# Kernel optimization log

Measured on AMD Instinct MI355X. Metric: run time of the kernel, lower is better.

## Reference

```python
import jax, jax.numpy as jnp
import numpy as np

EMBED_DIM = 384
ROUTER_HIDDEN = 64
NUM_EXPERTS = 4
TOP_K = 1
TEMPERATURE = 2.0  # buffer value, clamp(min=0.1) is a no-op here
LN_EPS = 1e-5


def setup_inputs() -> dict:
    key = jax.random.key(0)
    kx, k1, k2 = jax.random.split(key, 3)
    x = jax.random.normal(kx, (16, 8192, EMBED_DIM), dtype=jnp.float32)
    ln_w = jnp.ones((EMBED_DIM,), dtype=jnp.float32)
    ln_b = jnp.zeros((EMBED_DIM,), dtype=jnp.float32)
    # kaiming-uniform-ish init, scale irrelevant for correctness testing
    w1 = jax.random.normal(k1, (EMBED_DIM, ROUTER_HIDDEN), dtype=jnp.float32) / np.sqrt(EMBED_DIM)
    w2 = jax.random.normal(k2, (ROUTER_HIDDEN, NUM_EXPERTS), dtype=jnp.float32) / np.sqrt(ROUTER_HIDDEN)
    return {"x": x, "ln_w": ln_w, "ln_b": ln_b, "w1": w1, "w2": w2}


def reference(x, ln_w, ln_b, w1, w2):
    T = jnp.maximum(jnp.float32(TEMPERATURE), 0.1)
    # LayerNorm over last dim
    mu = jnp.mean(x, axis=-1, keepdims=True)
    var = jnp.mean(jnp.square(x - mu), axis=-1, keepdims=True)
    h = (x - mu) * jax.lax.rsqrt(var + LN_EPS) * ln_w + ln_b
    # MLP gate: Linear(384->64, no bias) -> GELU(exact) -> Linear(64->4, no bias)
    h = jax.nn.gelu(jnp.einsum("bld,dh->blh", h, w1), approximate=False)
    logits = jnp.einsum("blh,he->ble", h, w2) / T
    probs = jax.nn.softmax(logits, axis=-1)  # (B, L, E)
    _, indices = jax.lax.top_k(probs, TOP_K)  # (B, L, top_k)
    B, L = indices.shape[0], indices.shape[1]
    # load-balance aux loss (f is non-differentiable, as under torch.no_grad)
    one_hot = jax.nn.one_hot(indices, NUM_EXPERTS, dtype=jnp.float32)  # (B, L, K, E)
    f = jnp.sum(one_hot, axis=(0, 1, 2)) / (B * L * TOP_K)  # (E,)
    P = jnp.mean(probs, axis=(0, 1))  # (E,)
    aux_loss = NUM_EXPERTS * jnp.sum(f * P)
    return probs, indices, aux_loss, probs
```

## Files before the change

### kernel.cpp

```cpp
#include <hip/hip_runtime.h>
#include <math.h>

#define EMBED 384
#define HID 64
#define NE 4
#define TPB 512
#define MT 8
#define JS 8
#define JPT 8
#define TOKB 512

#define WLN_F   (EMBED * HID)
#define W2_OFF  (WLN_F)
#define C1_OFF  (W2_OFF + HID * NE)
#define C2_OFF  (C1_OFF + HID)
#define PART_OFF (C2_OFF + HID)
#define RED_OFF (PART_OFF + 2 * TPB)
#define SMEM_FLOATS (RED_OFF + 2 * NE)

__global__ void
__attribute__((amdgpu_flat_work_group_size(TPB, TPB), amdgpu_waves_per_eu(2, 2)))
router_main(
    const float* __restrict__ x, const float* __restrict__ lnw,
    const float* __restrict__ lnb, const float* __restrict__ w1,
    const float* __restrict__ w2, float* __restrict__ out,
    float* __restrict__ ws, int ntok)
{
  extern __shared__ float smem[];
  float* wln = smem;
  float* w2s = smem + W2_OFF;
  float* c1s = smem + C1_OFF;
  float* c2s = smem + C2_OFF;
  float* part = smem + PART_OFF;
  float* red = smem + RED_OFF;

  const int tid = (int)threadIdx.x;

  {
    const float4* src = reinterpret_cast<const float4*>(w1);
    float4* dst = reinterpret_cast<float4*>(wln);
    #pragma unroll
    for (int k = 0; k < (WLN_F / 4) / TPB; ++k) {
      const int f4 = tid + k * TPB;
      const float sc = lnw[f4 >> 4];
      float4 v = src[f4];
      v.x *= sc; v.y *= sc; v.z *= sc; v.w *= sc;
      dst[f4] = v;
    }
  }
  if (tid < HID * NE / 4) {
    reinterpret_cast<float4*>(w2s)[tid] = reinterpret_cast<const float4*>(w2)[tid];
  }
  if (tid < 2 * NE) red[tid] = 0.f;
  __syncthreads();

  {
    const int j = tid & 63;
    const int dpart = tid >> 6;
    float c1p = 0.f, c2p = 0.f;
    #pragma unroll 8
    for (int k = 0; k < EMBED / 8; ++k) {
      const int d = dpart * (EMBED / 8) + k;
      c1p += wln[d * HID + j];
      c2p = fmaf(lnb[d], w1[d * HID + j], c2p);
    }
    part[dpart * 64 + j] = c1p;
    part[TPB + dpart * 64 + j] = c2p;
  }
  __syncthreads();
  if (tid < HID) {
    float a = 0.f, b = 0.f;
    #pragma unroll
    for (int p = 0; p < 8; ++p) {
      a += part[p * 64 + tid];
      b += part[TPB + p * 64 + tid];
    }
    c1s[tid] = a;
    c2s[tid] = b;
  }
  __syncthreads();

  const int lane = tid & 63;
  const int wv = tid >> 6;
  const int tg = lane >> 3;
  const int jg = lane & 7;
  const int wbase = (int)blockIdx.x * TOKB + wv * 64;
  const int t0 = wbase + tg * MT;
  const int joff = jg * JPT;

  const float* __restrict__ xrow = x + (size_t)t0 * EMBED;

  float acc[MT][JPT];
  #pragma unroll
  for (int m = 0; m < MT; ++m)
    #pragma unroll
    for (int j = 0; j < JPT; ++j) acc[m][j] = 0.f;
  float s[MT], s2[MT];
  #pragma unroll
  for (int m = 0; m < MT; ++m) { s[m] = 0.f; s2[m] = 0.f; }

  #pragma unroll 2
  for (int dq = 0; dq < EMBED / 4; ++dq) {
    const int d = dq * 4;
    float4 xv[MT];
    #pragma unroll
    for (int m = 0; m < MT; ++m)
      xv[m] = *reinterpret_cast<const float4*>(xrow + (size_t)m * EMBED + d);
    #pragma unroll
    for (int m = 0; m < MT; ++m) {
      s[m] += (xv[m].x + xv[m].y) + (xv[m].z + xv[m].w);
      s2[m] = fmaf(xv[m].x, xv[m].x, s2[m]);
      s2[m] = fmaf(xv[m].y, xv[m].y, s2[m]);
      s2[m] = fmaf(xv[m].z, xv[m].z, s2[m]);
      s2[m] = fmaf(xv[m].w, xv[m].w, s2[m]);
    }
    #pragma unroll
    for (int dd = 0; dd < 4; ++dd) {
      const float* wr = wln + (d + dd) * HID + joff;
      float4 wa = *reinterpret_cast<const float4*>(wr);
      float4 wb = *reinterpret_cast<const float4*>(wr + 4);
      #pragma unroll
      for (int m = 0; m < MT; ++m) {
        const float xx = (dd == 0) ? xv[m].x : (dd == 1) ? xv[m].y
                       : (dd == 2) ? xv[m].z : xv[m].w;
        acc[m][0] = fmaf(xx, wa.x, acc[m][0]);
        acc[m][1] = fmaf(xx, wa.y, acc[m][1]);
        acc[m][2] = fmaf(xx, wa.z, acc[m][2]);
        acc[m][3] = fmaf(xx, wa.w, acc[m][3]);
        acc[m][4] = fmaf(xx, wb.x, acc[m][4]);
        acc[m][5] = fmaf(xx, wb.y, acc[m][5]);
        acc[m][6] = fmaf(xx, wb.z, acc[m][6]);
        acc[m][7] = fmaf(xx, wb.w, acc[m][7]);
      }
    }
  }

  float mu[MT], rstd[MT];
  #pragma unroll
  for (int m = 0; m < MT; ++m) {
    mu[m] = s[m] * (1.f / EMBED);
    const float var = fmaf(-mu[m], mu[m], s2[m] * (1.f / EMBED));
    rstd[m] = rsqrtf(var + 1e-5f);
  }

  float logit[MT][NE];
  #pragma unroll
  for (int m = 0; m < MT; ++m)
    #pragma unroll
    for (int e = 0; e < NE; ++e) logit[m][e] = 0.f;

  #pragma unroll
  for (int jj = 0; jj < JPT; ++jj) {
    const int j = joff + jj;
    const float c1 = c1s[j];
    const float c2 = c2s[j];
    float4 wv = *reinterpret_cast<const float4*>(w2s + j * NE);
    #pragma unroll
    for (int m = 0; m < MT; ++m) {
      const float hid = fmaf(rstd[m], fmaf(-mu[m], c1, acc[m][jj]), c2);
      const float g = 0.5f * hid * (1.f + erff(hid * 0.7071067811865475f));
      logit[m][0] = fmaf(g, wv.x, logit[m][0]);
      logit[m][1] = fmaf(g, wv.y, logit[m][1]);
      logit[m][2] = fmaf(g, wv.z, logit[m][2]);
      logit[m][3] = fmaf(g, wv.w, logit[m][3]);
    }
  }

  #pragma unroll
  for (int m = 0; m < MT; ++m)
    #pragma unroll
    for (int e = 0; e < NE; ++e) {
      logit[m][e] += __shfl_xor(logit[m][e], 1);
      logit[m][e] += __shfl_xor(logit[m][e], 2);
      logit[m][e] += __shfl_xor(logit[m][e], 4);
    }

  float l[NE];
  #pragma unroll
  for (int e = 0; e < NE; ++e) {
    float v = logit[0][e];
    v = (jg == 1) ? logit[1][e] : v;
    v = (jg == 2) ? logit[2][e] : v;
    v = (jg == 3) ? logit[3][e] : v;
    v = (jg == 4) ? logit[4][e] : v;
    v = (jg == 5) ? logit[5][e] : v;
    v = (jg == 6) ? logit[6][e] : v;
    v = (jg == 7) ? logit[7][e] : v;
    l[e] = v * 0.5f;
  }
  const int mytok = wbase + lane;

  const float mx = fmaxf(fmaxf(l[0], l[1]), fmaxf(l[2], l[3]));
  const float e0 = expf(l[0] - mx), e1 = expf(l[1] - mx),
              e2 = expf(l[2] - mx), e3 = expf(l[3] - mx);
  const float inv = 1.f / (e0 + e1 + e2 + e3);
  const float p0 = e0 * inv, p1 = e1 * inv, p2 = e2 * inv, p3 = e3 * inv;

  int best = 0; float bp = p0;
  if (p1 > bp) { bp = p1; best = 1; }
  if (p2 > bp) { bp = p2; best = 2; }
  if (p3 > bp) { bp = p3; best = 3; }

  if (mytok < ntok) {
    *reinterpret_cast<float4*>(out + (size_t)mytok * 4) = make_float4(p0, p1, p2, p3);
    out[(size_t)ntok * 4 + mytok] = (float)best;
    float* o3 = out + (size_t)ntok * 5 + 1 + (size_t)mytok * 4;
    o3[0] = p0; o3[1] = p1; o3[2] = p2; o3[3] = p3;
  }

  float psum[NE] = {p0, p1, p2, p3};
  float pcnt[NE];
  pcnt[0] = (best == 0) ? 1.f : 0.f;
  pcnt[1] = (best == 1) ? 1.f : 0.f;
  pcnt[2] = (best == 2) ? 1.f : 0.f;
  pcnt[3] = (best == 3) ? 1.f : 0.f;

  #pragma unroll
  for (int e = 0; e < NE; ++e) {
    float a = psum[e], c = pcnt[e];
    #pragma unroll
    for (int off = 32; off; off >>= 1) {
      a += __shfl_xor(a, off);
      c += __shfl_xor(c, off);
    }
    if (lane == 0) {
      atomicAdd(&red[e], a);
      atomicAdd(&red[NE + e], c);
    }
  }
  __syncthreads();
  if (tid < 2 * NE) atomicAdd(&ws[tid], red[tid]);
}

__global__ void router_finalize(const float* __restrict__ ws,
                                float* __restrict__ out, int ntok)
{
  if (threadIdx.x == 0 && blockIdx.x == 0) {
    const float invN = 1.f / (float)ntok;
    float aux = 0.f;
    #pragma unroll
    for (int e = 0; e < NE; ++e)
      aux = fmaf(ws[NE + e] * invN, ws[e] * invN, aux);
    out[(size_t)ntok * 5] = (float)NE * aux;
  }
}

extern "C" void kernel_launch(void* const* d_in, const int* in_sizes, int n_in,
                              void* d_out, int out_size, void* d_ws, size_t ws_size,
                              hipStream_t stream) {
  const float* x   = (const float*)d_in[0];
  const float* lnw = (const float*)d_in[1];
  const float* lnb = (const float*)d_in[2];
  const float* w1  = (const float*)d_in[3];
  const float* w2  = (const float*)d_in[4];
  float* out = (float*)d_out;
  float* ws  = (float*)d_ws;

  const int ntok = in_sizes[0] / EMBED;

  hipMemsetAsync(d_ws, 0, 2 * NE * sizeof(float), stream);

  const int blocks = (ntok + TOKB - 1) / TOKB;
  const size_t smem_bytes = SMEM_FLOATS * sizeof(float);
  router_main<<<blocks, TPB, smem_bytes, stream>>>(x, lnw, lnb, w1, w2, out, ws, ntok);
  router_finalize<<<1, 64, 0, stream>>>(ws, out, ntok);
}
```

Before: 128.9 us.

## Distribute LayerNorm stats across lanes and load x in float2 chunks

Each lane now computes the mean and variance statistics for a single token (its own row), and the results are broadcast to the group through shuffles. Before, every lane redundantly accumulated sums for all 8 tokens. The x loads for the GEMV are split into two float2 loads per dq step, which shrinks the live float4 register array, and the unroll-2 pragma is removed. The aim is to cut redundant ALU work and register pressure. The cost is extra global loads: each lane reads its own row separately, and the row reads are narrower.

```diff
diff --git a/kernel.cpp b/kernel.cpp
--- a/kernel.cpp
+++ b/kernel.cpp
@@ -89,58 +89,93 @@
   const int joff = jg * JPT;
 
   const float* __restrict__ xrow = x + (size_t)t0 * EMBED;
+  const float* __restrict__ xown = x + (size_t)(t0 + jg) * EMBED;
 
   float acc[MT][JPT];
   #pragma unroll
   for (int m = 0; m < MT; ++m)
     #pragma unroll
     for (int j = 0; j < JPT; ++j) acc[m][j] = 0.f;
-  float s[MT], s2[MT];
-  #pragma unroll
-  for (int m = 0; m < MT; ++m) { s[m] = 0.f; s2[m] = 0.f; }
-
-  #pragma unroll 2
+  float s = 0.f, s2 = 0.f;
+
   for (int dq = 0; dq < EMBED / 4; ++dq) {
     const int d = dq * 4;
-    float4 xv[MT];
-    #pragma unroll
-    for (int m = 0; m < MT; ++m)
-      xv[m] = *reinterpret_cast<const float4*>(xrow + (size_t)m * EMBED + d);
-    #pragma unroll
-    for (int m = 0; m < MT; ++m) {
-      s[m] += (xv[m].x + xv[m].y) + (xv[m].z + xv[m].w);
-      s2[m] = fmaf(xv[m].x, xv[m].x, s2[m]);
-      s2[m] = fmaf(xv[m].y, xv[m].y, s2[m]);
-      s2[m] = fmaf(xv[m].z, xv[m].z, s2[m]);
-      s2[m] = fmaf(xv[m].w, xv[m].w, s2[m]);
-    }
-    #pragma unroll
-    for (int dd = 0; dd < 4; ++dd) {
-      const float* wr = wln + (d + dd) * HID + joff;
-      float4 wa = *reinterpret_cast<const float4*>(wr);
-      float4 wb = *reinterpret_cast<const float4*>(wr + 4);
+
+    {
+      float4 xo = *reinterpret_cast<const float4*>(xown + d);
+      s += (xo.x + xo.y) + (xo.z + xo.w);
+      s2 = fmaf(xo.x, xo.x, s2);
+      s2 = fmaf(xo.y, xo.y, s2);
+      s2 = fmaf(xo.z, xo.z, s2);
+      s2 = fmaf(xo.w, xo.w, s2);
+    }
+
+    {
+      const float* wr = wln + d * HID + joff;
+      float4 wa0 = *reinterpret_cast<const float4*>(wr);
+      float4 wa1 = *reinterpret_cast<const float4*>(wr + 4);
+      float4 wb0 = *reinterpret_cast<const float4*>(wr + HID);
+      float4 wb1 = *reinterpret_cast<const float4*>(wr + HID + 4);
       #pragma unroll
       for (int m = 0; m < MT; ++m) {
-        const float xx = (dd == 0) ? xv[m].x : (dd == 1) ? xv[m].y
-                       : (dd == 2) ? xv[m].z : xv[m].w;
-        acc[m][0] = fmaf(xx, wa.x, acc[m][0]);
-        acc[m][1] = fmaf(xx, wa.y, acc[m][1]);
-        acc[m][2] = fmaf(xx, wa.z, acc[m][2]);
-        acc[m][3] = fmaf(xx, wa.w, acc[m][3]);
-        acc[m][4] = fmaf(xx, wb.x, acc[m][4]);
-        acc[m][5] = fmaf(xx, wb.y, acc[m][5]);
-        acc[m][6] = fmaf(xx, wb.z, acc[m][6]);
-        acc[m][7] = fmaf(xx, wb.w, acc[m][7]);
+        float2 xv = *reinterpret_cast<const float2*>(xrow + (size_t)m * EMBED + d);
+        acc[m][0] = fmaf(xv.x, wa0.x, acc[m][0]);
+        acc[m][1] = fmaf(xv.x, wa0.y, acc[m][1]);
+        acc[m][2] = fmaf(xv.x, wa0.z, acc[m][2]);
+        acc[m][3] = fmaf(xv.x, wa0.w, acc[m][3]);
+        acc[m][4] = fmaf(xv.x, wa1.x, acc[m][4]);
+        acc[m][5] = fmaf(xv.x, wa1.y, acc[m][5]);
+        acc[m][6] = fmaf(xv.x, wa1.z, acc[m][6]);
+        acc[m][7] = fmaf(xv.x, wa1.w, acc[m][7]);
+        acc[m][0] = fmaf(xv.y, wb0.x, acc[m][0]);
+        acc[m][1] = fmaf(xv.y, wb0.y, acc[m][1]);
+        acc[m][2] = fmaf(xv.y, wb0.z, acc[m][2]);
+        acc[m][3] = fmaf(xv.y, wb0.w, acc[m][3]);
+        acc[m][4] = fmaf(xv.y, wb1.x, acc[m][4]);
+        acc[m][5] = fmaf(xv.y, wb1.y, acc[m][5]);
+        acc[m][6] = fmaf(xv.y, wb1.z, acc[m][6]);
+        acc[m][7] = fmaf(xv.y, wb1.w, acc[m][7]);
       }
     }
-  }
-
+    {
+      const float* wr = wln + (d + 2) * HID + joff;
+      float4 wa0 = *reinterpret_cast<const float4*>(wr);
+      float4 wa1 = *reinterpret_cast<const float4*>(wr + 4);
+      float4 wb0 = *reinterpret_cast<const float4*>(wr + HID);
+      float4 wb1 = *reinterpret_cast<const float4*>(wr + HID + 4);
+      #pragma unroll
+      for (int m = 0; m < MT; ++m) {
+        float2 xv = *reinterpret_cast<const float2*>(xrow + (size_t)m * EMBED + d + 2);
+        acc[m][0] = fmaf(xv.x, wa0.x, acc[m][0]);
+        acc[m][1] = fmaf(xv.x, wa0.y, acc[m][1]);
+        acc[m][2] = fmaf(xv.x, wa0.z, acc[m][2]);
+        acc[m][3] = fmaf(xv.x, wa0.w, acc[m][3]);
+        acc[m][4] = fmaf(xv.x, wa1.x, acc[m][4]);
+        acc[m][5] = fmaf(xv.x, wa1.y, acc[m][5]);
+        acc[m][6] = fmaf(xv.x, wa1.z, acc[m][6]);
+        acc[m][7] = fmaf(xv.x, wa1.w, acc[m][7]);
+        acc[m][0] = fmaf(xv.y, wb0.x, acc[m][0]);
+        acc[m][1] = fmaf(xv.y, wb0.y, acc[m][1]);
+        acc[m][2] = fmaf(xv.y, wb0.z, acc[m][2]);
+        acc[m][3] = fmaf(xv.y, wb0.w, acc[m][3]);
+        acc[m][4] = fmaf(xv.y, wb1.x, acc[m][4]);
+        acc[m][5] = fmaf(xv.y, wb1.y, acc[m][5]);
+        acc[m][6] = fmaf(xv.y, wb1.z, acc[m][6]);
+        acc[m][7] = fmaf(xv.y, wb1.w, acc[m][7]);
+      }
+    }
+  }
+
+  const float mu_own = s * (1.f / EMBED);
+  const float var_own = fmaf(-mu_own, mu_own, s2 * (1.f / EMBED));
+  const float rstd_own = rsqrtf(var_own + 1e-5f);
+
+  const int gbase = lane & ~7;
   float mu[MT], rstd[MT];
   #pragma unroll
   for (int m = 0; m < MT; ++m) {
-    mu[m] = s[m] * (1.f / EMBED);
-    const float var = fmaf(-mu[m], mu[m], s2[m] * (1.f / EMBED));
-    rstd[m] = rsqrtf(var + 1e-5f);
+    mu[m]   = __shfl(mu_own,   gbase + m);
+    rstd[m] = __shfl(rstd_own, gbase + m);
   }
 
   float logit[MT][NE];
```

Result: no change. 127.1 us (-1.4%).
